# Kernel tuning notes

Hardware: AMD Instinct MI355X
Metric: run time of the kernel (lower is better)

Reference implementation:

```python
import jax, jax.numpy as jnp
import numpy as np


def setup_inputs() -> dict:
    key = jax.random.key(0)
    ks = jax.random.split(key, 7)
    B, I, H = 8192, 1024, 1024
    x = jax.random.normal(ks[0], (B, I), dtype=jnp.float32)
    h_prev = jax.random.normal(ks[1], (B, H), dtype=jnp.float32)
    C_prev = jax.random.normal(ks[2], (B, H), dtype=jnp.float32)
    W_f = jax.random.normal(ks[3], (I + H, H), dtype=jnp.float32) * 0.01
    W_i = jax.random.normal(ks[4], (I + H, H), dtype=jnp.float32) * 0.01
    W_C = jax.random.normal(ks[5], (I + H, H), dtype=jnp.float32) * 0.01
    W_o = jax.random.normal(ks[6], (I + H, H), dtype=jnp.float32) * 0.01
    b = jnp.zeros((H,), dtype=jnp.float32)
    return {"x": x, "h_prev": h_prev, "C_prev": C_prev,
            "W_f": W_f, "b_f": b, "W_i": W_i, "b_i": b,
            "W_C": W_C, "b_C": b, "W_o": W_o, "b_o": b}


def reference(x, h_prev, C_prev, W_f, b_f, W_i, b_i, W_C, b_C, W_o, b_o):
    combined = jnp.concatenate([x, h_prev], axis=1)  # [B, I+H]
    # Fuse the four gate GEMMs into one [B, I+H] x [I+H, 4H] matmul.
    W = jnp.concatenate([W_f, W_i, W_o, W_C], axis=1)  # [I+H, 4H]
    b = jnp.concatenate([b_f, b_i, b_o, b_C], axis=0)  # [4H]
    gates = combined @ W + b                            # [B, 4H]
    H = C_prev.shape[1]
    f_t = jax.nn.sigmoid(gates[:, 0:H])
    i_t = jax.nn.sigmoid(gates[:, H:2 * H])
    o_t = jax.nn.sigmoid(gates[:, 2 * H:3 * H])
    C_tilda = jnp.tanh(gates[:, 3 * H:4 * H])
    C_t = f_t * C_prev + i_t * C_tilda
    h_t = o_t * jnp.tanh(C_t)
    return (h_t, C_t)
```

## Files before the change

kernel.cpp:

```cpp
#include <hip/hip_runtime.h>
#include <hip/hip_bf16.h>

#define B_SZ 8192
#define IH   2048
#define H_SZ 1024
#define BM   256
#define BNF  128
#define BK   64
#define NT   (IH / BK)
#define ABYTES (BM * BK * 2)
#define WBYTES (BNF * BK * 2)
#define BUFB   (ABYTES + WBYTES)
#define LDS_TOT (3 * BUFB)

typedef __attribute__((ext_vector_type(8))) short  short8;
typedef __attribute__((ext_vector_type(4))) float  floatx4;

static __device__ __forceinline__ ushort f2bf(float f) {
  union { float f; unsigned u; } v; v.f = f;
  unsigned u = v.u;
  u += 0x7fffu + ((u >> 16) & 1u);
  return (ushort)(u >> 16);
}

static __device__ __forceinline__ float sigmoidf_(float x) {
  return 1.0f / (1.0f + __expf(-x));
}
static __device__ __forceinline__ float tanhf_(float x) {
  float ax = fabsf(x);
  float e = __expf(-2.0f * ax);
  float t = (1.0f - e) / (1.0f + e);
  return copysignf(t, x);
}

static __device__ __forceinline__ void gload_lds16(const void* gsrc, void* ldst) {
  __builtin_amdgcn_global_load_lds(
      (__attribute__((address_space(1))) const void*)gsrc,
      (__attribute__((address_space(3))) void*)ldst, 16, 0, 0);
}

__global__ __launch_bounds__(256) void convert_w_kernel(
    const float* __restrict__ Wf, const float* __restrict__ Wi,
    const float* __restrict__ Wo, const float* __restrict__ Wc,
    ushort* __restrict__ Wt) {
  __shared__ float tile[64][65];
  const int g  = blockIdx.z;
  const float* W = (g == 0) ? Wf : (g == 1) ? Wi : (g == 2) ? Wo : Wc;
  const int n0 = blockIdx.x * 64;
  const int k0 = blockIdx.y * 64;
  const int tid = threadIdx.x;
#pragma unroll
  for (int i = 0; i < 4; ++i) {
    int c = i * 256 + tid;
    int r = c >> 4, c4 = c & 15;
    float4 v = *(const float4*)(W + (size_t)(k0 + r) * H_SZ + n0 + c4 * 4);
    tile[r][c4 * 4 + 0] = v.x;
    tile[r][c4 * 4 + 1] = v.y;
    tile[r][c4 * 4 + 2] = v.z;
    tile[r][c4 * 4 + 3] = v.w;
  }
  __syncthreads();
  const int n  = tid >> 2;
  const int kc = (tid & 3) * 16;
  ushort o[16] __attribute__((aligned(16)));
#pragma unroll
  for (int e = 0; e < 16; ++e) o[e] = f2bf(tile[kc + e][n]);
  ushort* dst = Wt + ((size_t)g * H_SZ + n0 + n) * IH + k0 + kc;
  *(uint4*)(dst)     = *(uint4*)&o[0];
  *(uint4*)(dst + 8) = *(uint4*)&o[8];
}

__global__ __launch_bounds__(256) void convert_a_kernel(
    const float* __restrict__ x, const float* __restrict__ hp,
    ushort* __restrict__ Abf) {
  size_t idx = ((size_t)blockIdx.x * 256 + threadIdx.x) * 8;
  size_t row = idx >> 11;
  size_t col = idx & 2047;
  const float* src = (col < 1024) ? (x  + row * 1024 + col)
                                  : (hp + row * 1024 + (col - 1024));
  float4 v0 = *(const float4*)(src);
  float4 v1 = *(const float4*)(src + 4);
  ushort o[8] __attribute__((aligned(16)));
  o[0] = f2bf(v0.x); o[1] = f2bf(v0.y); o[2] = f2bf(v0.z); o[3] = f2bf(v0.w);
  o[4] = f2bf(v1.x); o[5] = f2bf(v1.y); o[6] = f2bf(v1.z); o[7] = f2bf(v1.w);
  *(uint4*)(Abf + idx) = *(uint4*)&o[0];
}

__global__ __launch_bounds__(512, 2) void lstm_fused_kernel(
    const float* __restrict__ Cp, const ushort* __restrict__ Wt,
    const ushort* __restrict__ Abf,
    const float* __restrict__ bf_, const float* __restrict__ bi_,
    const float* __restrict__ bo_, const float* __restrict__ bc_,
    float* __restrict__ out) {
  __shared__ char lds[LDS_TOT];

  const int bid = blockIdx.x;
  const int wg  = (bid & 7) * 128 + (bid >> 3);
  const int b0  = (wg >> 5) * BM;
  const int n0g = (wg & 31) * 32;

  const int tid = threadIdx.x;
  const int ln  = tid & 63;
  const int wv  = tid >> 6;

  floatx4 acc[2][8];
#pragma unroll
  for (int i = 0; i < 2; ++i)
#pragma unroll
    for (int j = 0; j < 8; ++j) acc[i][j] = {0.f, 0.f, 0.f, 0.f};

  auto stage = [&](char* bufp, int k0_) {
#pragma unroll
    for (int i = 0; i < 4; ++i) {
      int s  = i * 512 + tid;
      int r  = s >> 3;
      int kc = s & 7;
      const char* src = (const char*)Abf +
          ((size_t)(b0 + r) * IH + k0_) * 2 + ((kc * 16) ^ ((r & 7) << 4));
      gload_lds16(src, bufp + (i * 512 + wv * 64) * 16);
    }
    char* wbp = bufp + ABYTES;
#pragma unroll
    for (int i = 0; i < 2; ++i) {
      int s   = i * 512 + tid;
      int nrt = s >> 3;
      int kc  = s & 7;
      const char* src = (const char*)Wt +
          (((size_t)(nrt >> 5) * H_SZ + n0g + (nrt & 31)) * IH + k0_) * 2 +
          ((kc * 16) ^ ((nrt & 7) << 4));
      gload_lds16(src, wbp + (i * 512 + wv * 64) * 16);
    }
  };

  auto compute_tile = [&](const char* bufp) {
    const char* ab  = bufp;
    const char* wbp = bufp + ABYTES;
#pragma unroll
    for (int ks = 0; ks < 2; ++ks) {
      int kb = ks * 64 + ((ln >> 4) << 4);
      short8 aF[2];
#pragma unroll
      for (int mf = 0; mf < 2; ++mf) {
        int row = wv * 32 + mf * 16 + (ln & 15);
        aF[mf] = *(const short8*)(ab + row * 128 + (kb ^ ((row & 7) << 4)));
      }
#pragma unroll
      for (int j = 0; j < 8; ++j) {
        int nrt = j * 16 + (ln & 15);
        short8 bF = *(const short8*)(wbp + nrt * 128 + (kb ^ ((nrt & 7) << 4)));
        acc[0][j] = __builtin_amdgcn_mfma_f32_16x16x32_bf16(aF[0], bF, acc[0][j], 0, 0, 0);
        acc[1][j] = __builtin_amdgcn_mfma_f32_16x16x32_bf16(aF[1], bF, acc[1][j], 0, 0, 0);
      }
    }
  };

  stage(lds + 0 * BUFB, 0 * BK);
  stage(lds + 1 * BUFB, 1 * BK);
  asm volatile("s_waitcnt vmcnt(6)" ::: "memory");
  __builtin_amdgcn_s_barrier();
  __builtin_amdgcn_sched_barrier(0);

  int oc = 0;
  int os = 2 * BUFB;
#pragma unroll 1
  for (int t = 0; t < NT - 2; ++t) {
    stage(lds + os, (t + 2) * BK);
    compute_tile(lds + oc);
    asm volatile("s_waitcnt vmcnt(6)" ::: "memory");
    __builtin_amdgcn_s_barrier();
    __builtin_amdgcn_sched_barrier(0);
    oc += BUFB; if (oc == LDS_TOT) oc = 0;
    os += BUFB; if (os == LDS_TOT) os = 0;
  }
  compute_tile(lds + oc);
  asm volatile("s_waitcnt vmcnt(0)" ::: "memory");
  __builtin_amdgcn_s_barrier();
  __builtin_amdgcn_sched_barrier(0);
  oc += BUFB; if (oc == LDS_TOT) oc = 0;
  compute_tile(lds + oc);

  const int colq = ln & 15;
  const int rq   = ln >> 4;
  float* outh = out;
  float* outC = out + (size_t)B_SZ * H_SZ;
#pragma unroll
  for (int mf = 0; mf < 2; ++mf) {
#pragma unroll
    for (int ns = 0; ns < 2; ++ns) {
      int n = n0g + ns * 16 + colq;
      float vbf = bf_[n], vbi = bi_[n], vbo = bo_[n], vbc = bc_[n];
#pragma unroll
      for (int r = 0; r < 4; ++r) {
        int row = b0 + wv * 32 + mf * 16 + rq * 4 + r;
        float fg = sigmoidf_(acc[mf][0 + ns][r] + vbf);
        float ig = sigmoidf_(acc[mf][2 + ns][r] + vbi);
        float og = sigmoidf_(acc[mf][4 + ns][r] + vbo);
        float cg = tanhf_  (acc[mf][6 + ns][r] + vbc);
        float cp = Cp[(size_t)row * H_SZ + n];
        float Ct = fg * cp + ig * cg;
        float ht = og * tanhf_(Ct);
        outh[(size_t)row * H_SZ + n] = ht;
        outC[(size_t)row * H_SZ + n] = Ct;
      }
    }
  }
}

extern "C" void kernel_launch(void* const* d_in, const int* in_sizes, int n_in,
                              void* d_out, int out_size, void* d_ws, size_t ws_size,
                              hipStream_t stream) {
  const float* x  = (const float*)d_in[0];
  const float* hp = (const float*)d_in[1];
  const float* Cp = (const float*)d_in[2];
  const float* Wf = (const float*)d_in[3];
  const float* bf = (const float*)d_in[4];
  const float* Wi = (const float*)d_in[5];
  const float* bi = (const float*)d_in[6];
  const float* Wc = (const float*)d_in[7];
  const float* bc = (const float*)d_in[8];
  const float* Wo = (const float*)d_in[9];
  const float* bo = (const float*)d_in[10];

  ushort* Wt  = (ushort*)d_ws;
  ushort* Abf = (ushort*)((char*)d_ws + (16u << 20));

  dim3 gridT(16, 32, 4);
  convert_w_kernel<<<gridT, 256, 0, stream>>>(Wf, Wi, Wo, Wc, Wt);
  convert_a_kernel<<<8192, 256, 0, stream>>>(x, hp, Abf);

  lstm_fused_kernel<<<1024, 512, 0, stream>>>(Cp, Wt, Abf,
                                              bf, bi, bo, bc, (float*)d_out);
}
```

Baseline: 177.4 us.

## Enlarge GEMM tile to 256x256 with ping-pong LDS and interleaved MFMA/staging schedule

Each workgroup's tile grows from 256x128 (32 hidden units) to 256x256 (64 hidden units across four gates), which halves the grid to 512 blocks and doubles per-wave accumulators to 4x8. The triple-buffered 64-K pipeline becomes a two-buffer ping-pong of 128 KB LDS per block. Global-to-LDS staging is split into quarter chunks and interleaved with MFMA quadrants, separated by barriers and s_setprio. The goal is higher arithmetic intensity and overlap of loads with MFMA work. In exchange it uses more registers and LDS, leaving one block per CU, and adds many more barriers.

```diff
diff --git a/kernel.cpp b/kernel.cpp
--- a/kernel.cpp
+++ b/kernel.cpp
@@ -5,13 +5,11 @@
 #define IH   2048
 #define H_SZ 1024
 #define BM   256
-#define BNF  128
 #define BK   64
 #define NT   (IH / BK)
-#define ABYTES (BM * BK * 2)
-#define WBYTES (BNF * BK * 2)
-#define BUFB   (ABYTES + WBYTES)
-#define LDS_TOT (3 * BUFB)
+#define NI   (NT / 2)
+#define DBUF 65536
+#define WOFF 32768
 
 typedef __attribute__((ext_vector_type(8))) short  short8;
 typedef __attribute__((ext_vector_type(4))) float  floatx4;
@@ -22,7 +20,6 @@
   u += 0x7fffu + ((u >> 16) & 1u);
   return (ushort)(u >> 16);
 }
-
 static __device__ __forceinline__ float sigmoidf_(float x) {
   return 1.0f / (1.0f + __expf(-x));
 }
@@ -32,7 +29,6 @@
   float t = (1.0f - e) / (1.0f + e);
   return copysignf(t, x);
 }
-
 static __device__ __forceinline__ void gload_lds16(const void* gsrc, void* ldst) {
   __builtin_amdgcn_global_load_lds(
       (__attribute__((address_space(1))) const void*)gsrc,
@@ -92,106 +88,158 @@
     const float* __restrict__ bf_, const float* __restrict__ bi_,
     const float* __restrict__ bo_, const float* __restrict__ bc_,
     float* __restrict__ out) {
-  __shared__ char lds[LDS_TOT];
+  __shared__ char lds[2 * DBUF];
 
   const int bid = blockIdx.x;
-  const int wg  = (bid & 7) * 128 + (bid >> 3);
-  const int b0  = (wg >> 5) * BM;
-  const int n0g = (wg & 31) * 32;
+  const int wg  = (bid & 7) * 64 + (bid >> 3);
+  const int b0  = (wg >> 4) * BM;
+  const int n0g = (wg & 15) * 64;
 
   const int tid = threadIdx.x;
   const int ln  = tid & 63;
   const int wv  = tid >> 6;
-
-  floatx4 acc[2][8];
+  const int wm  = wv >> 1, wn = wv & 1;
+
+  floatx4 acc[4][8];
+#pragma unroll
+  for (int m = 0; m < 4; ++m)
+#pragma unroll
+    for (int j = 0; j < 8; ++j) acc[m][j] = {0.f, 0.f, 0.f, 0.f};
+
+  const int sw = (ln & 7) << 4;
+  int kb[2];
+  kb[0] = (((ln >> 4) << 4)) ^ sw;
+  kb[1] = (64 + ((ln >> 4) << 4)) ^ sw;
+  int arow[4], brow[8];
+#pragma unroll
+  for (int mf = 0; mf < 4; ++mf)
+    arow[mf] = (wm * 64 + mf * 16 + (ln & 15)) * 128;
+#pragma unroll
+  for (int j = 0; j < 8; ++j) {
+    int g = j >> 1, ns = j & 1;
+    brow[j] = WOFF + (g * 64 + wn * 32 + ns * 16 + (ln & 15)) * 128;
+  }
+
+  const int    kcsw = ((tid & 7) * 16) ^ (((tid >> 3) & 7) << 4);
+  const char*  AbfB = (const char*)Abf;
+  const char*  WtB  = (const char*)Wt;
+  size_t aoff[2];
 #pragma unroll
   for (int i = 0; i < 2; ++i)
-#pragma unroll
-    for (int j = 0; j < 8; ++j) acc[i][j] = {0.f, 0.f, 0.f, 0.f};
-
-  auto stage = [&](char* bufp, int k0_) {
-#pragma unroll
-    for (int i = 0; i < 4; ++i) {
-      int s  = i * 512 + tid;
-      int r  = s >> 3;
-      int kc = s & 7;
-      const char* src = (const char*)Abf +
-          ((size_t)(b0 + r) * IH + k0_) * 2 + ((kc * 16) ^ ((r & 7) << 4));
-      gload_lds16(src, bufp + (i * 512 + wv * 64) * 16);
+    aoff[i] = ((size_t)(b0 + i * 64 + (tid >> 3)) << 12) + kcsw;
+  size_t woff[2][2];
+#pragma unroll
+  for (int h = 0; h < 2; ++h)
+#pragma unroll
+    for (int i = 0; i < 2; ++i) {
+      int nrt  = h * 128 + i * 64 + (tid >> 3);
+      int g    = nrt >> 6, nloc = nrt & 63;
+      woff[h][i] = ((size_t)(g * H_SZ + n0g + nloc) << 12) + kcsw;
     }
-    char* wbp = bufp + ABYTES;
-#pragma unroll
-    for (int i = 0; i < 2; ++i) {
-      int s   = i * 512 + tid;
-      int nrt = s >> 3;
-      int kc  = s & 7;
-      const char* src = (const char*)Wt +
-          (((size_t)(nrt >> 5) * H_SZ + n0g + (nrt & 31)) * IH + k0_) * 2 +
-          ((kc * 16) ^ ((nrt & 7) << 4));
-      gload_lds16(src, wbp + (i * 512 + wv * 64) * 16);
-    }
-  };
-
-  auto compute_tile = [&](const char* bufp) {
-    const char* ab  = bufp;
-    const char* wbp = bufp + ABYTES;
-#pragma unroll
-    for (int ks = 0; ks < 2; ++ks) {
-      int kb = ks * 64 + ((ln >> 4) << 4);
-      short8 aF[2];
-#pragma unroll
-      for (int mf = 0; mf < 2; ++mf) {
-        int row = wv * 32 + mf * 16 + (ln & 15);
-        aF[mf] = *(const short8*)(ab + row * 128 + (kb ^ ((row & 7) << 4)));
-      }
-#pragma unroll
-      for (int j = 0; j < 8; ++j) {
-        int nrt = j * 16 + (ln & 15);
-        short8 bF = *(const short8*)(wbp + nrt * 128 + (kb ^ ((nrt & 7) << 4)));
-        acc[0][j] = __builtin_amdgcn_mfma_f32_16x16x32_bf16(aF[0], bF, acc[0][j], 0, 0, 0);
-        acc[1][j] = __builtin_amdgcn_mfma_f32_16x16x32_bf16(aF[1], bF, acc[1][j], 0, 0, 0);
-      }
-    }
-  };
-
-  stage(lds + 0 * BUFB, 0 * BK);
-  stage(lds + 1 * BUFB, 1 * BK);
-  asm volatile("s_waitcnt vmcnt(6)" ::: "memory");
-  __builtin_amdgcn_s_barrier();
-  __builtin_amdgcn_sched_barrier(0);
-
-  int oc = 0;
-  int os = 2 * BUFB;
+  int dsto[2];
+#pragma unroll
+  for (int i = 0; i < 2; ++i) dsto[i] = (i * 512 + wv * 64) * 16;
+
+#define STAGE_A(db, ktb, h)                                                   \
+  do {                                                                        \
+    gload_lds16(AbfB + aoff[0] + ((size_t)(h) << 19) + (ktb),                 \
+                lds + (db) + (h) * 16384 + dsto[0]);                          \
+    gload_lds16(AbfB + aoff[1] + ((size_t)(h) << 19) + (ktb),                 \
+                lds + (db) + (h) * 16384 + dsto[1]);                          \
+  } while (0)
+#define STAGE_W(db, ktb, h)                                                   \
+  do {                                                                        \
+    gload_lds16(WtB + woff[h][0] + (ktb),                                     \
+                lds + (db) + WOFF + (h) * 16384 + dsto[0]);                   \
+    gload_lds16(WtB + woff[h][1] + (ktb),                                     \
+                lds + (db) + WOFF + (h) * 16384 + dsto[1]);                   \
+  } while (0)
+
+  short8 aF[4][2];
+  short8 bF[8][2];
+#define RD_A(db, mf)                                                          \
+  do {                                                                        \
+    aF[mf][0] = *(const short8*)(lds + (db) + arow[mf] + kb[0]);              \
+    aF[mf][1] = *(const short8*)(lds + (db) + arow[mf] + kb[1]);              \
+  } while (0)
+#define RD_B(db, j)                                                           \
+  do {                                                                        \
+    bF[j][0] = *(const short8*)(lds + (db) + brow[j] + kb[0]);                \
+    bF[j][1] = *(const short8*)(lds + (db) + brow[j] + kb[1]);                \
+  } while (0)
+#define MFQ(mh, jh)                                                           \
+  do {                                                                        \
+    __builtin_amdgcn_s_setprio(1);                                            \
+    _Pragma("unroll")                                                         \
+    for (int mf_ = 2 * (mh); mf_ < 2 * (mh) + 2; ++mf_)                       \
+      _Pragma("unroll")                                                       \
+      for (int j_ = 4 * (jh); j_ < 4 * (jh) + 4; ++j_) {                      \
+        acc[mf_][j_] = __builtin_amdgcn_mfma_f32_16x16x32_bf16(               \
+            aF[mf_][0], bF[j_][0], acc[mf_][j_], 0, 0, 0);                    \
+        acc[mf_][j_] = __builtin_amdgcn_mfma_f32_16x16x32_bf16(               \
+            aF[mf_][1], bF[j_][1], acc[mf_][j_], 0, 0, 0);                    \
+      }                                                                       \
+    __builtin_amdgcn_s_setprio(0);                                            \
+  } while (0)
+#define BAR   __builtin_amdgcn_s_barrier()
+#define LGKM0                                                                 \
+  do {                                                                        \
+    asm volatile("s_waitcnt lgkmcnt(0)" ::: "memory");                        \
+    __builtin_amdgcn_sched_barrier(0);                                        \
+  } while (0)
+#define VMC6  asm volatile("s_waitcnt vmcnt(6)" ::: "memory")
+
+  STAGE_W(0, 0, 0); STAGE_A(0, 0, 0); STAGE_A(0, 0, 1); STAGE_W(0, 0, 1);
+  STAGE_W(DBUF, 128, 0); STAGE_A(DBUF, 128, 0); STAGE_A(DBUF, 128, 1);
+  VMC6;
+  BAR;
+
 #pragma unroll 1
-  for (int t = 0; t < NT - 2; ++t) {
-    stage(lds + os, (t + 2) * BK);
-    compute_tile(lds + oc);
-    asm volatile("s_waitcnt vmcnt(6)" ::: "memory");
-    __builtin_amdgcn_s_barrier();
-    __builtin_amdgcn_sched_barrier(0);
-    oc += BUFB; if (oc == LDS_TOT) oc = 0;
-    os += BUFB; if (os == LDS_TOT) os = 0;
-  }
-  compute_tile(lds + oc);
-  asm volatile("s_waitcnt vmcnt(0)" ::: "memory");
-  __builtin_amdgcn_s_barrier();
-  __builtin_amdgcn_sched_barrier(0);
-  oc += BUFB; if (oc == LDS_TOT) oc = 0;
-  compute_tile(lds + oc);
+  for (int it = 0; it < NI; ++it) {
+    const int kt1b  = (2 * it + 1) * 128;
+    const int ktn0b = ((2 * it + 2) & 31) * 128;
+    const int ktn1b = ((2 * it + 3) & 31) * 128;
+    RD_A(0, 0); RD_A(0, 1);
+    RD_B(0, 0); RD_B(0, 1); RD_B(0, 2); RD_B(0, 3);
+    STAGE_W(DBUF, kt1b, 1);
+    BAR; LGKM0; MFQ(0, 0); BAR;
+    RD_A(0, 2); RD_A(0, 3);
+    STAGE_W(0, ktn0b, 0);
+    BAR; LGKM0; MFQ(1, 0); BAR;
+    RD_B(0, 4); RD_B(0, 5); RD_B(0, 6); RD_B(0, 7);
+    STAGE_A(0, ktn0b, 0);
+    BAR; LGKM0; MFQ(0, 1); BAR;
+    STAGE_A(0, ktn0b, 1);
+    BAR; LGKM0; MFQ(1, 1);
+    VMC6; BAR;
+    RD_A(DBUF, 0); RD_A(DBUF, 1);
+    RD_B(DBUF, 0); RD_B(DBUF, 1); RD_B(DBUF, 2); RD_B(DBUF, 3);
+    STAGE_W(0, ktn0b, 1);
+    BAR; LGKM0; MFQ(0, 0); BAR;
+    RD_A(DBUF, 2); RD_A(DBUF, 3);
+    STAGE_W(DBUF, ktn1b, 0);
+    BAR; LGKM0; MFQ(1, 0); BAR;
+    RD_B(DBUF, 4); RD_B(DBUF, 5); RD_B(DBUF, 6); RD_B(DBUF, 7);
+    STAGE_A(DBUF, ktn1b, 0);
+    BAR; LGKM0; MFQ(0, 1); BAR;
+    STAGE_A(DBUF, ktn1b, 1);
+    BAR; LGKM0; MFQ(1, 1);
+    VMC6; BAR;
+  }
 
   const int colq = ln & 15;
   const int rq   = ln >> 4;
   float* outh = out;
   float* outC = out + (size_t)B_SZ * H_SZ;
 #pragma unroll
-  for (int mf = 0; mf < 2; ++mf) {
+  for (int mf = 0; mf < 4; ++mf) {
 #pragma unroll
     for (int ns = 0; ns < 2; ++ns) {
-      int n = n0g + ns * 16 + colq;
+      int n = n0g + wn * 32 + ns * 16 + colq;
       float vbf = bf_[n], vbi = bi_[n], vbo = bo_[n], vbc = bc_[n];
 #pragma unroll
       for (int r = 0; r < 4; ++r) {
-        int row = b0 + wv * 32 + mf * 16 + rq * 4 + r;
+        int row = b0 + wm * 64 + mf * 16 + rq * 4 + r;
         float fg = sigmoidf_(acc[mf][0 + ns][r] + vbf);
         float ig = sigmoidf_(acc[mf][2 + ns][r] + vbi);
         float og = sigmoidf_(acc[mf][4 + ns][r] + vbo);
@@ -204,6 +252,14 @@
       }
     }
   }
+#undef STAGE_A
+#undef STAGE_W
+#undef RD_A
+#undef RD_B
+#undef MFQ
+#undef BAR
+#undef LGKM0
+#undef VMC6
 }
 
 extern "C" void kernel_launch(void* const* d_in, const int* in_sizes, int n_in,
@@ -228,6 +284,6 @@
   convert_w_kernel<<<gridT, 256, 0, stream>>>(Wf, Wi, Wo, Wc, Wt);
   convert_a_kernel<<<8192, 256, 0, stream>>>(x, hp, Abf);
 
-  lstm_fused_kernel<<<1024, 512, 0, stream>>>(Cp, Wt, Abf,
-                                              bf, bi, bo, bc, (float*)d_out);
-}
+  lstm_fused_kernel<<<512, 512, 0, stream>>>(Cp, Wt, Abf,
+                                             bf, bi, bo, bc, (float*)d_out);
+}
```

After: 168.8 us. -4.8%, faster.
